# Optimization experiments

Hardware: AMD Instinct MI355X
Metric: run time of the kernel (lower is better)

The kernel has to match this reference:

```python
import jax, jax.numpy as jnp
import numpy as np
from jax import lax

N = 20000; E = 640000
D_IN = 64; F1 = 256; H = 256
HEADS = 8; HC = 128; DH = HC // HEADS
NA = 8; MS = 64


def setup_inputs() -> dict:
    key = jax.random.key(0)
    ks = jax.random.split(key, 40)
    def w(k, shape, fan):
        return (jax.random.normal(k, shape, jnp.float32) / np.sqrt(fan)).astype(jnp.float32)
    inp = {}
    inp['state'] = jax.random.normal(ks[0], (N, D_IN), jnp.float32)
    inp['message'] = jax.random.normal(ks[1], (N, MS), jnp.float32)
    inp['edge_index'] = jax.random.randint(ks[2], (2, E), 0, N)
    # fc1 / fc2
    inp['W_fc1'] = w(ks[3], (D_IN, F1), D_IN); inp['b_fc1'] = jnp.zeros((F1,), jnp.float32)
    inp['W_fc2'] = w(ks[4], (MS, F1), MS);    inp['b_fc2'] = jnp.zeros((F1,), jnp.float32)
    # GRU: 2 layers, torch layout W_ih [3H, in], W_hh [3H, H]
    inp['Wih0'] = w(ks[5], (3 * H, F1), F1); inp['Whh0'] = w(ks[6], (3 * H, H), H)
    inp['bih0'] = jnp.zeros((3 * H,), jnp.float32); inp['bhh0'] = jnp.zeros((3 * H,), jnp.float32)
    inp['Wih1'] = w(ks[7], (3 * H, H), H); inp['Whh1'] = w(ks[8], (3 * H, H), H)
    inp['bih1'] = jnp.zeros((3 * H,), jnp.float32); inp['bhh1'] = jnp.zeros((3 * H,), jnp.float32)
    # GAT layer 1: in H -> HEADS heads of DH (concat -> HC)
    inp['Wg1'] = w(ks[9], (H, HC), H)
    inp['as1'] = w(ks[10], (HEADS, DH), DH); inp['ad1'] = w(ks[11], (HEADS, DH), DH)
    inp['bg1'] = jnp.zeros((HC,), jnp.float32)
    # GAT layer 2: HC -> HC
    inp['Wg2'] = w(ks[12], (HC, HC), HC)
    inp['as2'] = w(ks[13], (HEADS, DH), DH); inp['ad2'] = w(ks[14], (HEADS, DH), DH)
    inp['bg2'] = jnp.zeros((HC,), jnp.float32)
    # heads
    inp['Wc'] = w(ks[15], (HC, 1), HC); inp['bc'] = jnp.zeros((1,), jnp.float32)
    inp['Wmu'] = w(ks[16], (HC + H, NA), HC + H); inp['bmu'] = jnp.zeros((NA,), jnp.float32)
    inp['Wm'] = w(ks[17], (HC, MS), HC); inp['bm'] = jnp.zeros((MS,), jnp.float32)
    return inp


def gru_layer(x_seq, Wih, Whh, bih, bhh):
    # x_seq: [N, in]; torch GRUCell math, batch size 1 squeezed
    h_dim = Whh.shape[1]
    def step(h, x):
        gi = x @ Wih.T + bih
        gh = h @ Whh.T + bhh
        ir, iz, inn = jnp.split(gi, 3)
        hr, hz, hn = jnp.split(gh, 3)
        r = jax.nn.sigmoid(ir + hr)
        z = jax.nn.sigmoid(iz + hz)
        n = jnp.tanh(inn + r * hn)
        h_new = (1.0 - z) * n + z * h
        return h_new, h_new
    h0 = jnp.zeros((h_dim,), x_seq.dtype)
    _, ys = lax.scan(step, h0, x_seq)
    return ys  # [N, h_dim]


def gat_conv(x, W, a_src, a_dst, b, src, dst):
    # x: [N, in] -> [N, HEADS*DH], edge softmax over incoming edges per dst node
    n = x.shape[0]
    h = (x @ W).reshape(n, HEADS, DH)
    e_src = jnp.einsum('nhd,hd->nh', h, a_src)  # [N, HEADS]
    e_dst = jnp.einsum('nhd,hd->nh', h, a_dst)
    e = jax.nn.leaky_relu(e_src[src] + e_dst[dst], 0.2)  # [E, HEADS]
    emax = jax.ops.segment_max(e, dst, num_segments=n)
    emax = lax.stop_gradient(jnp.where(jnp.isfinite(emax), emax, 0.0))
    p = jnp.exp(e - emax[dst])
    denom = jax.ops.segment_sum(p, dst, num_segments=n)
    alpha = p / (denom[dst] + 1e-16)  # [E, HEADS]
    msgs = h[src] * alpha[:, :, None]  # [E, HEADS, DH]
    out = jax.ops.segment_sum(msgs, dst, num_segments=n)
    return out.reshape(n, HEADS * DH) + b


def reference(state, message, edge_index, W_fc1, b_fc1, W_fc2, b_fc2,
              Wih0, Whh0, bih0, bhh0, Wih1, Whh1, bih1, bhh1,
              Wg1, as1, ad1, bg1, Wg2, as2, ad2, bg2,
              Wc, bc, Wmu, bmu, Wm, bm):
    src, dst = edge_index[0], edge_index[1]
    x = jax.nn.relu(state @ W_fc1 + b_fc1)          # [N, F1]
    m = jax.nn.relu(message @ W_fc2 + b_fc2)        # [N, F1]
    x = x + m
    x = gru_layer(x, Wih0, Whh0, bih0, bhh0)        # [N, H]
    x = gru_layer(x, Wih1, Whh1, bih1, bhh1)
    x = jax.nn.relu(x)
    xg = gat_conv(x, Wg1, as1, ad1, bg1, src, dst)  # [N, HC]
    xg = jax.nn.relu(xg)
    xg = gat_conv(xg, Wg2, as2, ad2, bg2, src, dst)
    comm = jax.nn.sigmoid(xg @ Wc + bc)             # [N, 1]
    mu = jnp.tanh(jnp.concatenate([x, xg], axis=-1) @ Wmu + bmu)  # [N, NA]
    msg_out = jnp.tanh(xg @ Wm + bm)                # [N, MS]
    return comm, msg_out, mu
```

## Files before the change

kernel.cpp:

```cpp
#include <hip/hip_runtime.h>
#include <stdint.h>

#define N_NODES 20000
#define E_EDGES 640000
#define F1 256
#define HDIM 256
#define G3 768
#define HEADS 8
#define HC 128
#define DH 16
#define NA 8
#define MS 64

typedef _Float16 h2 __attribute__((ext_vector_type(2)));

__device__ __forceinline__ float fdot2(uint32_t a, uint32_t b, float c) {
#if __has_builtin(__builtin_amdgcn_fdot2)
  return __builtin_amdgcn_fdot2(__builtin_bit_cast(h2, a), __builtin_bit_cast(h2, b), c, false);
#else
  h2 x = __builtin_bit_cast(h2, a), y = __builtin_bit_cast(h2, b);
  return c + (float)x[0] * (float)y[0] + (float)x[1] * (float)y[1];
#endif
}

__device__ __forceinline__ float fexp2(float x) { return __builtin_amdgcn_exp2f(x); }
__device__ __forceinline__ float frcp(float x)  { return __builtin_amdgcn_rcpf(x); }
__device__ __forceinline__ float sigm(float x)  { return frcp(1.f + fexp2(-1.44269504f * x)); }
__device__ __forceinline__ float tanh_(float x) {
  x = fminf(20.f, fmaxf(-20.f, x));
  float t = fexp2(2.88539008f * x);
  return (t - 1.f) * frcp(t + 1.f);
}
__device__ __forceinline__ float leaky(float x) { return (x > 0.f) ? x : 0.2f * x; }
__device__ __forceinline__ unsigned fenc(float f) {
  unsigned u = __float_as_uint(f);
  return (u & 0x80000000u) ? ~u : (u | 0x80000000u);
}
__device__ __forceinline__ float fdec(unsigned u) {
  return __uint_as_float((u & 0x80000000u) ? (u ^ 0x80000000u) : ~u);
}

#define GF_BIAS 1
#define GF_RELU_OUT 2
#define GF_ACC 4
#define GF_RELU_A 8
#define GF_BT 16

template <int FLAGS>
__global__ __launch_bounds__(256) void gemm_k(const float* __restrict__ A,
                                              const float* __restrict__ B,
                                              const float* __restrict__ bias,
                                              float* __restrict__ C,
                                              int M, int K, int P) {
  __shared__ float As[64][68];
  __shared__ float Bs[64][68];
  int colTiles = P >> 6;
  int bx = blockIdx.x % colTiles;
  int by = blockIdx.x / colTiles;
  int row0 = by * 64, col0 = bx * 64;
  int tid = threadIdx.x;
  int tx = tid & 15, ty = tid >> 4;
  float acc[4][4] = {};
  for (int k0 = 0; k0 < K; k0 += 64) {
    {
      int r = tid >> 2, kq = (tid & 3) * 16;
      int gr = row0 + r;
      const float* ap = A + (size_t)gr * K + k0 + kq;
#pragma unroll
      for (int j = 0; j < 4; j++) {
        float4 v = make_float4(0.f, 0.f, 0.f, 0.f);
        if (gr < M) v = *(const float4*)(ap + 4 * j);
        if (FLAGS & GF_RELU_A) {
          v.x = fmaxf(v.x, 0.f); v.y = fmaxf(v.y, 0.f);
          v.z = fmaxf(v.z, 0.f); v.w = fmaxf(v.w, 0.f);
        }
        As[kq + 4 * j + 0][r] = v.x; As[kq + 4 * j + 1][r] = v.y;
        As[kq + 4 * j + 2][r] = v.z; As[kq + 4 * j + 3][r] = v.w;
      }
    }
    if (FLAGS & GF_BT) {
      int n = tid >> 2, kq = (tid & 3) * 16;
      const float* bp = B + (size_t)(col0 + n) * K + k0 + kq;
#pragma unroll
      for (int j = 0; j < 4; j++) {
        float4 v = *(const float4*)(bp + 4 * j);
        Bs[kq + 4 * j + 0][n] = v.x; Bs[kq + 4 * j + 1][n] = v.y;
        Bs[kq + 4 * j + 2][n] = v.z; Bs[kq + 4 * j + 3][n] = v.w;
      }
    } else {
      int kk = tid >> 2, nq = (tid & 3) * 16;
      const float* bp = B + (size_t)(k0 + kk) * P + col0 + nq;
#pragma unroll
      for (int j = 0; j < 4; j++)
        *(float4*)&Bs[kk][nq + 4 * j] = *(const float4*)(bp + 4 * j);
    }
    __syncthreads();
#pragma unroll
    for (int kk = 0; kk < 64; kk++) {
      float4 av = *(const float4*)&As[kk][ty * 4];
      float4 bv = *(const float4*)&Bs[kk][tx * 4];
      float a4[4] = {av.x, av.y, av.z, av.w};
      float b4[4] = {bv.x, bv.y, bv.z, bv.w};
#pragma unroll
      for (int i = 0; i < 4; i++)
#pragma unroll
        for (int j = 0; j < 4; j++) acc[i][j] = fmaf(a4[i], b4[j], acc[i][j]);
    }
    __syncthreads();
  }
#pragma unroll
  for (int i = 0; i < 4; i++) {
    int gr = row0 + ty * 4 + i;
    if (gr >= M) continue;
#pragma unroll
    for (int j = 0; j < 4; j++) {
      int gc = col0 + tx * 4 + j;
      float v = acc[i][j];
      if (FLAGS & GF_BIAS) v += bias[gc];
      if (FLAGS & GF_RELU_OUT) v = fmaxf(v, 0.f);
      size_t o = (size_t)gr * P + gc;
      if (FLAGS & GF_ACC) C[o] += v; else C[o] = v;
    }
  }
}

__global__ __launch_bounds__(256) void prep_w(const float* __restrict__ Whh,
                                              uint32_t* __restrict__ Wpk) {
  int idx = blockIdx.x * 256 + threadIdx.x;
  if (idx >= 48 * 2048) return;
  int i = idx >> 11;
  int rem = idx & 2047;
  int t = rem >> 2, comp = rem & 3;
  int q = 4 * i + comp;
  int g = t >> 2, c = t & 3;
  int a = q >> 5, p = q & 31;
  int row = (a % 3) * 256 + 2 * g + (a / 3);
  int k = 64 * c + 2 * p;
  h2 v = { (_Float16)Whh[row * 256 + k], (_Float16)Whh[row * 256 + k + 1] };
  Wpk[idx] = __builtin_bit_cast(uint32_t, v);
}

#define WD(i) uint4 W##i = Wp4[(i) * 512 + tid];
#define PIN(i) asm volatile("" : "+v"(W##i.x), "+v"(W##i.y), "+v"(W##i.z), "+v"(W##i.w));
#define DOT6(A,B,C,D,E,F, m, hv) \
  a0 = fdot2(A.m, hv, a0); a1 = fdot2(B.m, hv, a1); a2 = fdot2(C.m, hv, a2); \
  a3 = fdot2(D.m, hv, a3); a4 = fdot2(E.m, hv, a4); a5 = fdot2(F.m, hv, a5);
#define DOT4(H, A,B,C,D,E,F) \
  DOT6(A,B,C,D,E,F, x, H.x) DOT6(A,B,C,D,E,F, y, H.y) \
  DOT6(A,B,C,D,E,F, z, H.z) DOT6(A,B,C,D,E,F, w, H.w)

__global__ __launch_bounds__(512, 2) void gru_scan(const float* __restrict__ GI,
                                                   const uint32_t* __restrict__ Wpk,
                                                   const float* __restrict__ bhh,
                                                   float* __restrict__ Hout) {
  __shared__ __align__(16) uint32_t hb[2][4][36];
  int tid = threadIdx.x;
  int g = tid >> 2, c = tid & 3;
  int lane = tid & 63;
  const uint4* Wp4 = (const uint4*)Wpk;
  WD(0)  WD(1)  WD(2)  WD(3)  WD(4)  WD(5)  WD(6)  WD(7)
  WD(8)  WD(9)  WD(10) WD(11) WD(12) WD(13) WD(14) WD(15)
  WD(16) WD(17) WD(18) WD(19) WD(20) WD(21) WD(22) WD(23)
  WD(24) WD(25) WD(26) WD(27) WD(28) WD(29) WD(30) WD(31)
  WD(32) WD(33) WD(34) WD(35) WD(36) WD(37) WD(38) WD(39)
  WD(40) WD(41) WD(42) WD(43) WD(44) WD(45) WD(46) WD(47)
  PIN(0)  PIN(1)  PIN(2)  PIN(3)  PIN(4)  PIN(5)  PIN(6)  PIN(7)
  PIN(8)  PIN(9)  PIN(10) PIN(11) PIN(12) PIN(13) PIN(14) PIN(15)
  PIN(16) PIN(17) PIN(18) PIN(19) PIN(20) PIN(21) PIN(22) PIN(23)
  PIN(24) PIN(25) PIN(26) PIN(27) PIN(28) PIN(29) PIN(30) PIN(31)
  PIN(32) PIN(33) PIN(34) PIN(35) PIN(36) PIN(37) PIN(38) PIN(39)
  PIN(40) PIN(41) PIN(42) PIN(43) PIN(44) PIN(45) PIN(46) PIN(47)
  for (int i = tid; i < 2 * 4 * 36; i += 512) ((uint32_t*)hb)[i] = 0;
  bool gatel = ((c & 1) == 0);
  int j = 2 * g + (c >> 1);
  float bh_r = 0, bh_z = 0, bh_n = 0, hreg = 0, gr = 0, gz = 0, gn = 0;
  if (gatel) {
    bh_r = bhh[j]; bh_z = bhh[256 + j]; bh_n = bhh[512 + j];
    gr = GI[j]; gz = GI[256 + j]; gn = GI[512 + j];
  }
  __syncthreads();
  int buf = 0;
  const int bl = lane & ~3;
#pragma unroll 1
  for (int t = 0; t < N_NODES; t++) {
    float pgr = 0, pgz = 0, pgn = 0;
    if (gatel) {
      int tn = (t + 1 < N_NODES) ? t + 1 : t;
      const float* gp = GI + (size_t)tn * G3;
      pgr = gp[j]; pgz = gp[256 + j]; pgn = gp[512 + j];
    }
    float a0 = 0, a1 = 0, a2 = 0, a3 = 0, a4 = 0, a5 = 0;
    const uint4* hc4 = (const uint4*)(&hb[buf][c][0]);
    uint4 Ha = hc4[0];
    uint4 Hb = hc4[1];
    DOT4(Ha, W0, W8,  W16, W24, W32, W40)  Ha = hc4[2];
    DOT4(Hb, W1, W9,  W17, W25, W33, W41)  Hb = hc4[3];
    DOT4(Ha, W2, W10, W18, W26, W34, W42)  Ha = hc4[4];
    DOT4(Hb, W3, W11, W19, W27, W35, W43)  Hb = hc4[5];
    DOT4(Ha, W4, W12, W20, W28, W36, W44)  Ha = hc4[6];
    DOT4(Hb, W5, W13, W21, W29, W37, W45)  Hb = hc4[7];
    DOT4(Ha, W6, W14, W22, W30, W38, W46)
    DOT4(Hb, W7, W15, W23, W31, W39, W47)
    float v6 = 0.f, v7 = 0.f;
    float u0, u1, u2, u3;
    {
      float t0 = __shfl_xor(a0, 2, 64), t4 = __shfl_xor(a4, 2, 64);
      u0 = (c & 2) ? a4 + t4 : a0 + t0;
      float t1 = __shfl_xor(a1, 2, 64), t5 = __shfl_xor(a5, 2, 64);
      u1 = (c & 2) ? a5 + t5 : a1 + t1;
      float t2 = __shfl_xor(a2, 2, 64), t6 = __shfl_xor(v6, 2, 64);
      u2 = (c & 2) ? v6 + t6 : a2 + t2;
      float t3 = __shfl_xor(a3, 2, 64), t7 = __shfl_xor(v7, 2, 64);
      u3 = (c & 2) ? v7 + t7 : a3 + t3;
    }
    float f0, f1;
    {
      float t0 = __shfl_xor(u0, 1, 64), t2 = __shfl_xor(u2, 1, 64);
      f0 = (c & 1) ? u2 + t2 : u0 + t0;
      float t1 = __shfl_xor(u1, 1, 64), t3 = __shfl_xor(u3, 1, 64);
      f1 = (c & 1) ? u3 + t3 : u1 + t1;
    }
    float ta = __shfl(f0, bl + 1, 64);
    float tb = __shfl(f1, bl + 1, 64);
    if (gatel) {
      float Sr = (c == 0) ? f0 : tb;
      float Sz = (c == 0) ? f1 : f0;
      float Sn = (c == 0) ? ta : f1;
      float r = sigm(gr + bh_r + Sr);
      float z = sigm(gz + bh_z + Sz);
      float n = tanh_(gn + r * (Sn + bh_n));
      float hn = (1.f - z) * n + z * hreg;
      hreg = hn;
      Hout[(size_t)t * HDIM + j] = hn;
      int pj = j >> 1, cc = pj >> 5, half = j & 1;
      ushort* hw = (ushort*)&hb[buf ^ 1][cc][0];
      hw[(pj & 31) * 2 + half] = __builtin_bit_cast(uint16_t, (_Float16)hn);
      gr = pgr; gz = pgz; gn = pgn;
    }
    __syncthreads();
    buf ^= 1;
  }
}

__global__ __launch_bounds__(256) void esed_k(const float* __restrict__ Hg,
                                              const float* __restrict__ a_s,
                                              const float* __restrict__ a_d,
                                              float* __restrict__ es, float* __restrict__ ed) {
  int idx = blockIdx.x * 256 + threadIdx.x;
  if (idx >= N_NODES * HEADS) return;
  int n = idx >> 3, hd = idx & 7;
  const float* hp = Hg + (size_t)n * HC + hd * DH;
  float s = 0, d = 0;
#pragma unroll
  for (int i = 0; i < DH; i++) {
    float h = hp[i];
    s = fmaf(h, a_s[hd * DH + i], s);
    d = fmaf(h, a_d[hd * DH + i], d);
  }
  es[idx] = s; ed[idx] = d;
}

__global__ __launch_bounds__(256) void esmax_k(const float* __restrict__ es,
                                               unsigned* __restrict__ m) {
  int idx = blockIdx.x * 256 + threadIdx.x;
  float v = (idx < N_NODES * HEADS) ? es[idx] : -1e30f;
#pragma unroll
  for (int mask = 32; mask >= 8; mask >>= 1) v = fmaxf(v, __shfl_xor(v, mask, 64));
  if ((threadIdx.x & 63) < 8) atomicMax(&m[threadIdx.x & 7], fenc(v));
}

__global__ __launch_bounds__(256) void deg_k(const int* __restrict__ ei, int* __restrict__ deg) {
  int e = blockIdx.x * 256 + threadIdx.x;
  if (e >= E_EDGES) return;
  atomicAdd(&deg[ei[E_EDGES + e]], 1);
}

__global__ __launch_bounds__(1024) void scan_k(const int* __restrict__ deg, int* __restrict__ off) {
  __shared__ int wsum[16];
  __shared__ int carry;
  int tid = threadIdx.x, lane = tid & 63, wv = tid >> 6;
  if (tid == 0) carry = 0;
  __syncthreads();
  for (int base = 0; base < N_NODES; base += 1024) {
    int i = base + tid;
    int v = (i < N_NODES) ? deg[i] : 0;
    int s = v;
#pragma unroll
    for (int d = 1; d < 64; d <<= 1) {
      int t = __shfl_up(s, d, 64);
      if (lane >= d) s += t;
    }
    if (lane == 63) wsum[wv] = s;
    __syncthreads();
    if (wv == 0 && lane < 16) {
      int t = wsum[lane];
#pragma unroll
      for (int d = 1; d < 16; d <<= 1) {
        int u = __shfl_up(t, d, 64);
        if (lane >= d) t += u;
      }
      wsum[lane] = t;
    }
    __syncthreads();
    int prev = (wv > 0) ? wsum[wv - 1] : 0;
    int excl = carry + prev + s - v;
    if (i < N_NODES) off[i] = excl;
    int total = wsum[15];
    __syncthreads();
    if (tid == 0) carry += total;
    __syncthreads();
  }
  if (tid == 0) off[N_NODES] = carry;
}

__global__ __launch_bounds__(256) void scatter_k(const int* __restrict__ ei,
                                                 const int* __restrict__ off,
                                                 int* __restrict__ cnt,
                                                 int* __restrict__ csr_src) {
  int e = blockIdx.x * 256 + threadIdx.x;
  if (e >= E_EDGES) return;
  int d = ei[E_EDGES + e];
  int pos = off[d] + atomicAdd(&cnt[d], 1);
  csr_src[pos] = ei[e];
}

template <int RELU>
__global__ __launch_bounds__(256) void gather_k(const int* __restrict__ off,
                                                const int* __restrict__ csr_src,
                                                const float* __restrict__ es,
                                                const float* __restrict__ ed,
                                                const unsigned* __restrict__ esm,
                                                const float* __restrict__ Hg,
                                                const float* __restrict__ bias,
                                                float* __restrict__ out) {
  int wv = threadIdx.x >> 6, lane = threadIdx.x & 63;
  int d = blockIdx.x * 4 + wv;
  if (d >= N_NODES) return;
  int hd0 = lane >> 4, hd1 = 4 + (lane >> 4);
  float ed0 = ed[d * 8 + hd0], ed1 = ed[d * 8 + hd1];
  float cb0 = leaky(fdec(esm[hd0]) + ed0);
  float cb1 = leaky(fdec(esm[hd1]) + ed1);
  int e0 = off[d], e1 = off[d + 1];
  float acc0 = 0, acc1 = 0, den0 = 0, den1 = 0;
  for (int i = e0; i < e1; i++) {
    int s = csr_src[i];
    float p0 = fexp2(1.44269504f * (leaky(es[s * 8 + hd0] + ed0) - cb0));
    float p1 = fexp2(1.44269504f * (leaky(es[s * 8 + hd1] + ed1) - cb1));
    float h0 = Hg[(size_t)s * HC + lane];
    float h1 = Hg[(size_t)s * HC + 64 + lane];
    acc0 = fmaf(p0, h0, acc0); acc1 = fmaf(p1, h1, acc1);
    den0 += p0; den1 += p1;
  }
  float o0 = acc0 * frcp(den0 + 1e-16f);
  float o1 = acc1 * frcp(den1 + 1e-16f);
  if (RELU) {
    o0 = fmaxf(o0 + bias[lane], 0.f);
    o1 = fmaxf(o1 + bias[64 + lane], 0.f);
  }
  out[(size_t)d * HC + lane] = o0;
  out[(size_t)d * HC + 64 + lane] = o1;
}

__global__ __launch_bounds__(64) void heads_k(const float* __restrict__ xgb,
                                              const float* __restrict__ bg2,
                                              const float* __restrict__ H2,
                                              const float* __restrict__ Wc, const float* __restrict__ bc,
                                              const float* __restrict__ Wmu, const float* __restrict__ bmu,
                                              const float* __restrict__ Wm, const float* __restrict__ bm,
                                              float* __restrict__ out) {
  int n = blockIdx.x, l = threadIdx.x;
  __shared__ float xg[HC];
  __shared__ float xr[HDIM];
  for (int i = l; i < HC; i += 64) xg[i] = xgb[(size_t)n * HC + i] + bg2[i];
  for (int i = l; i < HDIM; i += 64) xr[i] = fmaxf(H2[(size_t)n * HDIM + i], 0.f);
  __syncthreads();
  float acc = bm[l];
#pragma unroll 8
  for (int k = 0; k < HC; k++) acc = fmaf(xg[k], Wm[k * MS + l], acc);
  out[N_NODES + (size_t)n * MS + l] = tanh_(acc);
  if (l < NA) {
    float a = bmu[l];
    for (int k = 0; k < HDIM; k++) a = fmaf(xr[k], Wmu[k * NA + l], a);
    for (int k = 0; k < HC; k++) a = fmaf(xg[k], Wmu[(HDIM + k) * NA + l], a);
    out[N_NODES + (size_t)N_NODES * MS + (size_t)n * NA + l] = tanh_(a);
  }
  if (l == 0) {
    float a = bc[0];
    for (int k = 0; k < HC; k++) a = fmaf(xg[k], Wc[k], a);
    out[n] = sigm(a);
  }
}

extern "C" void kernel_launch(void* const* d_in, const int* in_sizes, int n_in,
                              void* d_out, int out_size, void* d_ws, size_t ws_size,
                              hipStream_t stream) {
  const float* state = (const float*)d_in[0];
  const float* message = (const float*)d_in[1];
  const int* ei = (const int*)d_in[2];
  const float* Wfc1 = (const float*)d_in[3]; const float* bfc1 = (const float*)d_in[4];
  const float* Wfc2 = (const float*)d_in[5]; const float* bfc2 = (const float*)d_in[6];
  const float* Wih0 = (const float*)d_in[7]; const float* Whh0 = (const float*)d_in[8];
  const float* bih0 = (const float*)d_in[9]; const float* bhh0 = (const float*)d_in[10];
  const float* Wih1 = (const float*)d_in[11]; const float* Whh1 = (const float*)d_in[12];
  const float* bih1 = (const float*)d_in[13]; const float* bhh1 = (const float*)d_in[14];
  const float* Wg1 = (const float*)d_in[15]; const float* as1 = (const float*)d_in[16];
  const float* ad1 = (const float*)d_in[17]; const float* bg1 = (const float*)d_in[18];
  const float* Wg2 = (const float*)d_in[19]; const float* as2 = (const float*)d_in[20];
  const float* ad2 = (const float*)d_in[21]; const float* bg2 = (const float*)d_in[22];
  const float* Wc = (const float*)d_in[23]; const float* bc = (const float*)d_in[24];
  const float* Wmu = (const float*)d_in[25]; const float* bmu = (const float*)d_in[26];
  const float* Wm = (const float*)d_in[27]; const float* bm = (const float*)d_in[28];

  float* ws = (float*)d_ws;
  float* GI = ws;
  float* HGa = ws;
  float* HGb = ws + 2560000;
  float* X2  = ws + 5120000;
  float* ES  = ws + 7680000;
  float* ED  = ws + 7840000;
  unsigned* ESM = (unsigned*)(ws + 8160000);
  int* DEG = (int*)(ws + 8200000);
  int* OFF = (int*)(ws + 8230000);
  int* CNT = (int*)(ws + 8260000);
  int* CSR = (int*)(ws + 8300000);
  float* X  = ws + 15360000;
  float* H2 = ws + 20480000;
  uint32_t* Wpk = (uint32_t*)(ws + 25600000);
  float* out = (float*)d_out;

  int rt = (N_NODES + 63) / 64;

  gemm_k<GF_BIAS | GF_RELU_OUT><<<rt * 4, 256, 0, stream>>>(state, Wfc1, bfc1, X, N_NODES, 64, 256);
  gemm_k<GF_BIAS | GF_RELU_OUT | GF_ACC><<<rt * 4, 256, 0, stream>>>(message, Wfc2, bfc2, X, N_NODES, 64, 256);
  gemm_k<GF_BIAS | GF_BT><<<rt * 12, 256, 0, stream>>>(X, Wih0, bih0, GI, N_NODES, 256, G3);
  prep_w<<<384, 256, 0, stream>>>(Whh0, Wpk);
  gru_scan<<<1, 512, 0, stream>>>(GI, Wpk, bhh0, X);
  gemm_k<GF_BIAS | GF_BT><<<rt * 12, 256, 0, stream>>>(X, Wih1, bih1, GI, N_NODES, 256, G3);
  prep_w<<<384, 256, 0, stream>>>(Whh1, Wpk);
  gru_scan<<<1, 512, 0, stream>>>(GI, Wpk, bhh1, H2);
  hipMemsetAsync(DEG, 0, N_NODES * 4, stream);
  hipMemsetAsync(CNT, 0, N_NODES * 4, stream);
  deg_k<<<2500, 256, 0, stream>>>(ei, DEG);
  scan_k<<<1, 1024, 0, stream>>>(DEG, OFF);
  scatter_k<<<2500, 256, 0, stream>>>(ei, OFF, CNT, CSR);
  gemm_k<GF_RELU_A><<<rt * 2, 256, 0, stream>>>(H2, Wg1, nullptr, HGa, N_NODES, 256, HC);
  esed_k<<<625, 256, 0, stream>>>(HGa, as1, ad1, ES, ED);
  hipMemsetAsync(ESM, 0, 8 * 4, stream);
  esmax_k<<<625, 256, 0, stream>>>(ES, ESM);
  gather_k<1><<<5000, 256, 0, stream>>>(OFF, CSR, ES, ED, ESM, HGa, bg1, X2);
  gemm_k<0><<<rt * 2, 256, 0, stream>>>(X2, Wg2, nullptr, HGa, N_NODES, HC, HC);
  esed_k<<<625, 256, 0, stream>>>(HGa, as2, ad2, ES, ED);
  hipMemsetAsync(ESM, 0, 8 * 4, stream);
  esmax_k<<<625, 256, 0, stream>>>(ES, ESM);
  gather_k<0><<<5000, 256, 0, stream>>>(OFF, CSR, ES, ED, ESM, HGa, nullptr, HGb);
  heads_k<<<N_NODES, 64, 0, stream>>>(HGb, bg2, H2, Wc, bc, Wmu, bmu, Wm, bm, out);
}
```

Before: 51.93 ms.

## Split GRU recurrence over 1024 threads and fold r/z hidden biases into GEMM

The sequential GRU scan now uses 1024 threads, with each group of 4 lanes owning one hidden unit and accumulating its three gate dot products. That halves the per-thread fp16 dot2 chain and replaces the old multi-stage shuffle reduction with two xor-shuffles per gate. The packed Whh layout is reorganised to match. The r and z hidden biases are pre-added into the input-projection bias through a small prep kernel, which removes per-step bias adds. The scan is launched as 64 identical blocks where only block 0 writes output, so the other 63 blocks do redundant work.

```diff
diff --git a/kernel.cpp b/kernel.cpp
--- a/kernel.cpp
+++ b/kernel.cpp
@@ -127,116 +127,86 @@
 __global__ __launch_bounds__(256) void prep_w(const float* __restrict__ Whh,
                                               uint32_t* __restrict__ Wpk) {
   int idx = blockIdx.x * 256 + threadIdx.x;
-  if (idx >= 48 * 2048) return;
-  int i = idx >> 11;
-  int rem = idx & 2047;
+  if (idx >= 24 * 4096) return;
+  int i = idx >> 12;
+  int rem = idx & 4095;
   int t = rem >> 2, comp = rem & 3;
   int q = 4 * i + comp;
   int g = t >> 2, c = t & 3;
   int a = q >> 5, p = q & 31;
-  int row = (a % 3) * 256 + 2 * g + (a / 3);
+  int row = a * 256 + g;
   int k = 64 * c + 2 * p;
   h2 v = { (_Float16)Whh[row * 256 + k], (_Float16)Whh[row * 256 + k + 1] };
   Wpk[idx] = __builtin_bit_cast(uint32_t, v);
 }
 
-#define WD(i) uint4 W##i = Wp4[(i) * 512 + tid];
+__global__ __launch_bounds__(256) void prep_b(const float* __restrict__ bih,
+                                              const float* __restrict__ bhh,
+                                              float* __restrict__ b2) {
+  int i = blockIdx.x * 256 + threadIdx.x;
+  if (i < G3) b2[i] = bih[i] + (i < 512 ? bhh[i] : 0.f);
+}
+
+#define WD3(i) uint4 W##i = Wp4[(i) * 1024 + tid];
 #define PIN(i) asm volatile("" : "+v"(W##i.x), "+v"(W##i.y), "+v"(W##i.z), "+v"(W##i.w));
-#define DOT6(A,B,C,D,E,F, m, hv) \
-  a0 = fdot2(A.m, hv, a0); a1 = fdot2(B.m, hv, a1); a2 = fdot2(C.m, hv, a2); \
-  a3 = fdot2(D.m, hv, a3); a4 = fdot2(E.m, hv, a4); a5 = fdot2(F.m, hv, a5);
-#define DOT4(H, A,B,C,D,E,F) \
-  DOT6(A,B,C,D,E,F, x, H.x) DOT6(A,B,C,D,E,F, y, H.y) \
-  DOT6(A,B,C,D,E,F, z, H.z) DOT6(A,B,C,D,E,F, w, H.w)
-
-__global__ __launch_bounds__(512, 2) void gru_scan(const float* __restrict__ GI,
-                                                   const uint32_t* __restrict__ Wpk,
-                                                   const float* __restrict__ bhh,
-                                                   float* __restrict__ Hout) {
+#define DOT3x4(H, A, B, C2) \
+  s0 = fdot2(A.x, H.x, s0); s1 = fdot2(B.x, H.x, s1); s2 = fdot2(C2.x, H.x, s2); \
+  s0 = fdot2(A.y, H.y, s0); s1 = fdot2(B.y, H.y, s1); s2 = fdot2(C2.y, H.y, s2); \
+  s0 = fdot2(A.z, H.z, s0); s1 = fdot2(B.z, H.z, s1); s2 = fdot2(C2.z, H.z, s2); \
+  s0 = fdot2(A.w, H.w, s0); s1 = fdot2(B.w, H.w, s1); s2 = fdot2(C2.w, H.w, s2);
+
+__global__ __launch_bounds__(1024) void gru_scan(const float* __restrict__ GI,
+                                                 const uint32_t* __restrict__ Wpk,
+                                                 const float* __restrict__ bhh,
+                                                 float* __restrict__ Hout) {
   __shared__ __align__(16) uint32_t hb[2][4][36];
   int tid = threadIdx.x;
   int g = tid >> 2, c = tid & 3;
-  int lane = tid & 63;
   const uint4* Wp4 = (const uint4*)Wpk;
-  WD(0)  WD(1)  WD(2)  WD(3)  WD(4)  WD(5)  WD(6)  WD(7)
-  WD(8)  WD(9)  WD(10) WD(11) WD(12) WD(13) WD(14) WD(15)
-  WD(16) WD(17) WD(18) WD(19) WD(20) WD(21) WD(22) WD(23)
-  WD(24) WD(25) WD(26) WD(27) WD(28) WD(29) WD(30) WD(31)
-  WD(32) WD(33) WD(34) WD(35) WD(36) WD(37) WD(38) WD(39)
-  WD(40) WD(41) WD(42) WD(43) WD(44) WD(45) WD(46) WD(47)
+  WD3(0)  WD3(1)  WD3(2)  WD3(3)  WD3(4)  WD3(5)  WD3(6)  WD3(7)
+  WD3(8)  WD3(9)  WD3(10) WD3(11) WD3(12) WD3(13) WD3(14) WD3(15)
+  WD3(16) WD3(17) WD3(18) WD3(19) WD3(20) WD3(21) WD3(22) WD3(23)
   PIN(0)  PIN(1)  PIN(2)  PIN(3)  PIN(4)  PIN(5)  PIN(6)  PIN(7)
   PIN(8)  PIN(9)  PIN(10) PIN(11) PIN(12) PIN(13) PIN(14) PIN(15)
   PIN(16) PIN(17) PIN(18) PIN(19) PIN(20) PIN(21) PIN(22) PIN(23)
-  PIN(24) PIN(25) PIN(26) PIN(27) PIN(28) PIN(29) PIN(30) PIN(31)
-  PIN(32) PIN(33) PIN(34) PIN(35) PIN(36) PIN(37) PIN(38) PIN(39)
-  PIN(40) PIN(41) PIN(42) PIN(43) PIN(44) PIN(45) PIN(46) PIN(47)
-  for (int i = tid; i < 2 * 4 * 36; i += 512) ((uint32_t*)hb)[i] = 0;
-  bool gatel = ((c & 1) == 0);
-  int j = 2 * g + (c >> 1);
-  float bh_r = 0, bh_z = 0, bh_n = 0, hreg = 0, gr = 0, gz = 0, gn = 0;
-  if (gatel) {
-    bh_r = bhh[j]; bh_z = bhh[256 + j]; bh_n = bhh[512 + j];
-    gr = GI[j]; gz = GI[256 + j]; gn = GI[512 + j];
-  }
+  for (int i = tid; i < 2 * 4 * 36; i += 1024) ((uint32_t*)hb)[i] = 0;
+  bool wr = (blockIdx.x == 0);
+  float bh_n = bhh[512 + g];
+  float gr = GI[g], gz = GI[256 + g], gn = GI[512 + g];
+  float hreg = 0.f;
   __syncthreads();
   int buf = 0;
-  const int bl = lane & ~3;
 #pragma unroll 1
   for (int t = 0; t < N_NODES; t++) {
-    float pgr = 0, pgz = 0, pgn = 0;
-    if (gatel) {
-      int tn = (t + 1 < N_NODES) ? t + 1 : t;
-      const float* gp = GI + (size_t)tn * G3;
-      pgr = gp[j]; pgz = gp[256 + j]; pgn = gp[512 + j];
-    }
-    float a0 = 0, a1 = 0, a2 = 0, a3 = 0, a4 = 0, a5 = 0;
+    int tn = (t + 1 < N_NODES) ? t + 1 : t;
+    const float* gp = GI + (size_t)tn * G3;
+    float pgr = gp[g], pgz = gp[256 + g], pgn = gp[512 + g];
+    float s0 = 0.f, s1 = 0.f, s2 = 0.f;
     const uint4* hc4 = (const uint4*)(&hb[buf][c][0]);
-    uint4 Ha = hc4[0];
-    uint4 Hb = hc4[1];
-    DOT4(Ha, W0, W8,  W16, W24, W32, W40)  Ha = hc4[2];
-    DOT4(Hb, W1, W9,  W17, W25, W33, W41)  Hb = hc4[3];
-    DOT4(Ha, W2, W10, W18, W26, W34, W42)  Ha = hc4[4];
-    DOT4(Hb, W3, W11, W19, W27, W35, W43)  Hb = hc4[5];
-    DOT4(Ha, W4, W12, W20, W28, W36, W44)  Ha = hc4[6];
-    DOT4(Hb, W5, W13, W21, W29, W37, W45)  Hb = hc4[7];
-    DOT4(Ha, W6, W14, W22, W30, W38, W46)
-    DOT4(Hb, W7, W15, W23, W31, W39, W47)
-    float v6 = 0.f, v7 = 0.f;
-    float u0, u1, u2, u3;
-    {
-      float t0 = __shfl_xor(a0, 2, 64), t4 = __shfl_xor(a4, 2, 64);
-      u0 = (c & 2) ? a4 + t4 : a0 + t0;
-      float t1 = __shfl_xor(a1, 2, 64), t5 = __shfl_xor(a5, 2, 64);
-      u1 = (c & 2) ? a5 + t5 : a1 + t1;
-      float t2 = __shfl_xor(a2, 2, 64), t6 = __shfl_xor(v6, 2, 64);
-      u2 = (c & 2) ? v6 + t6 : a2 + t2;
-      float t3 = __shfl_xor(a3, 2, 64), t7 = __shfl_xor(v7, 2, 64);
-      u3 = (c & 2) ? v7 + t7 : a3 + t3;
-    }
-    float f0, f1;
-    {
-      float t0 = __shfl_xor(u0, 1, 64), t2 = __shfl_xor(u2, 1, 64);
-      f0 = (c & 1) ? u2 + t2 : u0 + t0;
-      float t1 = __shfl_xor(u1, 1, 64), t3 = __shfl_xor(u3, 1, 64);
-      f1 = (c & 1) ? u3 + t3 : u1 + t1;
-    }
-    float ta = __shfl(f0, bl + 1, 64);
-    float tb = __shfl(f1, bl + 1, 64);
-    if (gatel) {
-      float Sr = (c == 0) ? f0 : tb;
-      float Sz = (c == 0) ? f1 : f0;
-      float Sn = (c == 0) ? ta : f1;
-      float r = sigm(gr + bh_r + Sr);
-      float z = sigm(gz + bh_z + Sz);
-      float n = tanh_(gn + r * (Sn + bh_n));
-      float hn = (1.f - z) * n + z * hreg;
-      hreg = hn;
-      Hout[(size_t)t * HDIM + j] = hn;
-      int pj = j >> 1, cc = pj >> 5, half = j & 1;
+    uint4 Ha = hc4[0], Hb = hc4[1];
+    DOT3x4(Ha, W0, W8,  W16)  Ha = hc4[2];
+    DOT3x4(Hb, W1, W9,  W17)  Hb = hc4[3];
+    DOT3x4(Ha, W2, W10, W18)  Ha = hc4[4];
+    DOT3x4(Hb, W3, W11, W19)  Hb = hc4[5];
+    DOT3x4(Ha, W4, W12, W20)  Ha = hc4[6];
+    DOT3x4(Hb, W5, W13, W21)  Hb = hc4[7];
+    DOT3x4(Ha, W6, W14, W22)
+    DOT3x4(Hb, W7, W15, W23)
+    s0 += __shfl_xor(s0, 1, 64); s0 += __shfl_xor(s0, 2, 64);
+    s1 += __shfl_xor(s1, 1, 64); s1 += __shfl_xor(s1, 2, 64);
+    s2 += __shfl_xor(s2, 1, 64); s2 += __shfl_xor(s2, 2, 64);
+    float r = sigm(gr + s0);
+    float z = sigm(gz + s1);
+    float n = tanh_(gn + r * (s2 + bh_n));
+    float hn = (1.f - z) * n + z * hreg;
+    hreg = hn;
+    if (c == 0) {
+      if (wr) Hout[(size_t)t * HDIM + g] = hn;
+      int cc = g >> 6, v = g & 63, p = v >> 1, half = g & 1;
       ushort* hw = (ushort*)&hb[buf ^ 1][cc][0];
-      hw[(pj & 31) * 2 + half] = __builtin_bit_cast(uint16_t, (_Float16)hn);
-      gr = pgr; gz = pgz; gn = pgn;
-    }
+      hw[2 * p + half] = __builtin_bit_cast(uint16_t, (_Float16)hn);
+    }
+    gr = pgr; gz = pgz; gn = pgn;
     __syncthreads();
     buf ^= 1;
   }
@@ -425,6 +395,7 @@
   int* CSR = (int*)(ws + 8300000);
   float* X  = ws + 15360000;
   float* H2 = ws + 20480000;
+  float* B2  = H2;
   uint32_t* Wpk = (uint32_t*)(ws + 25600000);
   float* out = (float*)d_out;
 
@@ -432,12 +403,14 @@
 
   gemm_k<GF_BIAS | GF_RELU_OUT><<<rt * 4, 256, 0, stream>>>(state, Wfc1, bfc1, X, N_NODES, 64, 256);
   gemm_k<GF_BIAS | GF_RELU_OUT | GF_ACC><<<rt * 4, 256, 0, stream>>>(message, Wfc2, bfc2, X, N_NODES, 64, 256);
-  gemm_k<GF_BIAS | GF_BT><<<rt * 12, 256, 0, stream>>>(X, Wih0, bih0, GI, N_NODES, 256, G3);
+  prep_b<<<3, 256, 0, stream>>>(bih0, bhh0, B2);
+  gemm_k<GF_BIAS | GF_BT><<<rt * 12, 256, 0, stream>>>(X, Wih0, B2, GI, N_NODES, 256, G3);
   prep_w<<<384, 256, 0, stream>>>(Whh0, Wpk);
-  gru_scan<<<1, 512, 0, stream>>>(GI, Wpk, bhh0, X);
-  gemm_k<GF_BIAS | GF_BT><<<rt * 12, 256, 0, stream>>>(X, Wih1, bih1, GI, N_NODES, 256, G3);
+  gru_scan<<<64, 1024, 0, stream>>>(GI, Wpk, bhh0, X);
+  prep_b<<<3, 256, 0, stream>>>(bih1, bhh1, B2);
+  gemm_k<GF_BIAS | GF_BT><<<rt * 12, 256, 0, stream>>>(X, Wih1, B2, GI, N_NODES, 256, G3);
   prep_w<<<384, 256, 0, stream>>>(Whh1, Wpk);
-  gru_scan<<<1, 512, 0, stream>>>(GI, Wpk, bhh1, H2);
+  gru_scan<<<64, 1024, 0, stream>>>(GI, Wpk, bhh1, H2);
   hipMemsetAsync(DEG, 0, N_NODES * 4, stream);
   hipMemsetAsync(CNT, 0, N_NODES * 4, stream);
   deg_k<<<2500, 256, 0, stream>>>(ei, DEG);
```

Measured after the change: 56.17 ms. 1.08x slower.
